# Performance work log

Measured on AMD Instinct MI355X. Metric: run time of the kernel, lower is better.

The kernel has to match this reference:

```python
import jax, jax.numpy as jnp
import numpy as np

B = 256          # graphs per batch
NPG = 512        # nodes per data graph
NG = B * NPG     # 131072 data-graph nodes
EG = NG * 8      # 1048576 data-graph edges
NQPG = 16        # nodes per query graph
NQ = B * NQPG    # 4096 query nodes
EQ = NQ * 8      # 32768 query edges
IN, H, L, OUT = 64, 128, 2, 1


def setup_inputs() -> dict:
    key = jax.random.key(0)
    ks = jax.random.split(key, 24)
    # edges constrained within each graph (offset + local index)
    g_off = jnp.repeat(jnp.arange(B, dtype=jnp.int32) * NPG, EG // B)
    q_off = jnp.repeat(jnp.arange(B, dtype=jnp.int32) * NQPG, EQ // B)
    inp = {
        "X": jax.random.normal(ks[0], (NG, IN), jnp.float32),
        "X_q": jax.random.normal(ks[1], (NQ, IN), jnp.float32),
        "g_src": g_off + jax.random.randint(ks[2], (EG,), 0, NPG, jnp.int32),
        "g_dst": g_off + jax.random.randint(ks[3], (EG,), 0, NPG, jnp.int32),
        "g_n2g": jnp.repeat(jnp.arange(B, dtype=jnp.int32), NPG),
        "q_src": q_off + jax.random.randint(ks[4], (EQ,), 0, NQPG, jnp.int32),
        "q_dst": q_off + jax.random.randint(ks[5], (EQ,), 0, NQPG, jnp.int32),
        "q_n2g": jnp.repeat(jnp.arange(B, dtype=jnp.int32), NQPG),
    }
    def lin(k, fi, fo):
        s = 1.0 / np.sqrt(fi)
        return jax.random.uniform(k, (fi, fo), jnp.float32, -s, s)
    inp["Wg"] = lin(ks[6], IN, H); inp["bg"] = jnp.zeros((H,), jnp.float32)
    inp["Wq"] = lin(ks[7], IN, H); inp["bq"] = jnp.zeros((H,), jnp.float32)
    inp["betas_g"] = jnp.ones((L,), jnp.float32)  # AGNN beta, init 1
    inp["betas_q"] = jnp.ones((L,), jnp.float32)
    inp["W1r"] = jnp.stack([lin(jax.random.fold_in(ks[8], l), 2 * H, H) for l in range(L)])
    inp["b1r"] = jnp.zeros((L, H), jnp.float32)
    inp["W2r"] = jnp.stack([lin(jax.random.fold_in(ks[9], l), H, H) for l in range(L)])
    inp["b2r"] = jnp.zeros((L, H), jnp.float32)
    inp["Wp1"] = lin(ks[10], H, H); inp["bp1"] = jnp.zeros((H,), jnp.float32)
    inp["Wp2"] = lin(ks[11], H, OUT); inp["bp2"] = jnp.zeros((OUT,), jnp.float32)
    return inp


def agnn(h, src, dst, beta, n):
    # DGL AGNNConv: edge logit = beta * cos(h_dst, h_src); softmax over in-edges of dst;
    # output_i = sum_j alpha_ij * h_j. Nodes with no in-edges get zeros.
    hn = h * jax.lax.rsqrt(jnp.sum(h * h, -1, keepdims=True) + 1e-24)
    e = beta * jnp.sum(hn[src] * hn[dst], -1)                      # [E]
    m = jax.ops.segment_max(e, dst, num_segments=n)
    m = jnp.where(jnp.isfinite(m), m, 0.0)
    ee = jnp.exp(e - m[dst])
    den = jax.ops.segment_sum(ee, dst, num_segments=n)             # [N]
    num = jax.ops.segment_sum(ee[:, None] * h[src], dst, num_segments=n)
    return jnp.where(den[:, None] > 0, num / jnp.maximum(den, 1e-24)[:, None], 0.0)


def reference(X, X_q, g_src, g_dst, g_n2g, q_src, q_dst, q_n2g,
              Wg, bg, Wq, bq, betas_g, betas_q, W1r, b1r, W2r, b2r,
              Wp1, bp1, Wp2, bp2):
    h_g = X @ Wg + bg              # [NG, H]
    h_q = X_q @ Wq + bq            # [NQ, H]
    for l in range(L):
        h_q = agnn(h_q, q_src, q_dst, betas_q[l], NQ)
        h_q_aggr = jax.ops.segment_sum(h_q, q_n2g, num_segments=B)        # dgl.sum_nodes -> [B, H]
        h_cat = jnp.concatenate([h_g, h_q_aggr[g_n2g]], axis=-1)          # per-node broadcast, [NG, 2H]
        h = agnn(h_cat, g_src, g_dst, betas_g[l], NG)                     # [NG, 2H]
        h_g = jax.nn.relu(h @ W1r[l] + b1r[l]) @ W2r[l] + b2r[l]          # MLP reduce -> [NG, H]
    hg_sum = jax.ops.segment_sum(h_g, g_n2g, num_segments=B)             # sum-pool per graph
    y = jax.nn.relu(hg_sum @ Wp1 + bp1) @ Wp2 + bp2                       # SumPredictor -> [B, OUT]
    return y
```

## Files before the change

kernel.cpp:

```cpp
#include <hip/hip_runtime.h>
#include <stdint.h>

#define B_   256
#define NPG  512
#define NG   131072
#define EPG  4096
#define NQPG 16
#define NQ   4096
#define EQPG 128
#define L_   2
#define HPITCH 136

typedef __attribute__((ext_vector_type(8))) short short8;
typedef __attribute__((ext_vector_type(4))) float floatx4;

__device__ inline float bf2f(unsigned short u){
    union { unsigned int i; float f; } x; x.i = ((unsigned int)u) << 16; return x.f;
}
__device__ inline unsigned short f2bf(float f){
    union { float f; unsigned int i; } x; x.f = f;
    unsigned int r = x.i + 0x7fff + ((x.i >> 16) & 1);
    return (unsigned short)(r >> 16);
}
__device__ inline float d2(unsigned int a, unsigned int b, float c){
#if __has_builtin(__builtin_amdgcn_fdot2_f32_bf16)
    typedef __attribute__((ext_vector_type(2))) __bf16 bf16x2;
    union { unsigned int u; bf16x2 v; } xa, xb;
    xa.u = a; xb.u = b;
    return __builtin_amdgcn_fdot2_f32_bf16(xa.v, xb.v, c, false);
#else
    union { unsigned int u; float f; } la, ha, lb, hb;
    la.u = a << 16; ha.u = a & 0xffff0000u;
    lb.u = b << 16; hb.u = b & 0xffff0000u;
    return fmaf(la.f, lb.f, fmaf(ha.f, hb.f, c));
#endif
}
__device__ inline float dot8(uint4 a, uint4 b){
    return d2(a.x,b.x, d2(a.y,b.y, d2(a.z,b.z, d2(a.w,b.w, 0.f))));
}
__device__ inline float dot8q(uint4 a, uint4 b, float c0){
    return d2(a.x,b.x, d2(a.y,b.y, d2(a.z,b.z, d2(a.w,b.w, c0))));
}

#if __has_builtin(__builtin_amdgcn_exp2f)
#define FEXP2(x) __builtin_amdgcn_exp2f(x)
#else
#define FEXP2(x) __expf((x) * 0.6931471805599453f)
#endif
#define LOG2E_ 1.4426950408889634f

__device__ inline float red16dpp(float v){
#if __has_builtin(__builtin_amdgcn_mov_dpp)
    int i;
    i = __builtin_amdgcn_mov_dpp(__float_as_int(v), 0xB1, 0xF, 0xF, true);
    v += __int_as_float(i);
    i = __builtin_amdgcn_mov_dpp(__float_as_int(v), 0x4E, 0xF, 0xF, true);
    v += __int_as_float(i);
    i = __builtin_amdgcn_mov_dpp(__float_as_int(v), 0x141, 0xF, 0xF, true);
    v += __int_as_float(i);
    i = __builtin_amdgcn_mov_dpp(__float_as_int(v), 0x128, 0xF, 0xF, true);
    v += __int_as_float(i);
    return v;
#else
    v += __shfl_xor(v,1); v += __shfl_xor(v,2);
    v += __shfl_xor(v,4); v += __shfl_xor(v,8);
    return v;
#endif
}

__device__ inline void red16dpp4(float& v0, float& v1, float& v2, float& v3){
#if defined(__gfx950__) || defined(__gfx942__) || defined(__gfx90a__)
    asm volatile(
        "s_nop 1\n\t"
        "v_add_f32_dpp %0, %0, %0 quad_perm:[1,0,3,2] row_mask:0xf bank_mask:0xf\n\t"
        "v_add_f32_dpp %1, %1, %1 quad_perm:[1,0,3,2] row_mask:0xf bank_mask:0xf\n\t"
        "v_add_f32_dpp %2, %2, %2 quad_perm:[1,0,3,2] row_mask:0xf bank_mask:0xf\n\t"
        "v_add_f32_dpp %3, %3, %3 quad_perm:[1,0,3,2] row_mask:0xf bank_mask:0xf\n\t"
        "v_add_f32_dpp %0, %0, %0 quad_perm:[2,3,0,1] row_mask:0xf bank_mask:0xf\n\t"
        "v_add_f32_dpp %1, %1, %1 quad_perm:[2,3,0,1] row_mask:0xf bank_mask:0xf\n\t"
        "v_add_f32_dpp %2, %2, %2 quad_perm:[2,3,0,1] row_mask:0xf bank_mask:0xf\n\t"
        "v_add_f32_dpp %3, %3, %3 quad_perm:[2,3,0,1] row_mask:0xf bank_mask:0xf\n\t"
        "v_add_f32_dpp %0, %0, %0 row_half_mirror row_mask:0xf bank_mask:0xf\n\t"
        "v_add_f32_dpp %1, %1, %1 row_half_mirror row_mask:0xf bank_mask:0xf\n\t"
        "v_add_f32_dpp %2, %2, %2 row_half_mirror row_mask:0xf bank_mask:0xf\n\t"
        "v_add_f32_dpp %3, %3, %3 row_half_mirror row_mask:0xf bank_mask:0xf\n\t"
        "v_add_f32_dpp %0, %0, %0 row_ror:8 row_mask:0xf bank_mask:0xf\n\t"
        "v_add_f32_dpp %1, %1, %1 row_ror:8 row_mask:0xf bank_mask:0xf\n\t"
        "v_add_f32_dpp %2, %2, %2 row_ror:8 row_mask:0xf bank_mask:0xf\n\t"
        "v_add_f32_dpp %3, %3, %3 row_ror:8 row_mask:0xf bank_mask:0xf"
        : "+v"(v0), "+v"(v1), "+v"(v2), "+v"(v3));
#else
    v0 = red16dpp(v0); v1 = red16dpp(v1); v2 = red16dpp(v2); v3 = red16dpp(v3);
#endif
}

#define ACCUM8(p0,p1,p2,p3,p4,p5,p6,p7,e,u) do { \
    p0 = fmaf(e, bf2f((unsigned short)((u).x&0xffffu)), p0); \
    p1 = fmaf(e, bf2f((unsigned short)((u).x>>16)),    p1); \
    p2 = fmaf(e, bf2f((unsigned short)((u).y&0xffffu)), p2); \
    p3 = fmaf(e, bf2f((unsigned short)((u).y>>16)),    p3); \
    p4 = fmaf(e, bf2f((unsigned short)((u).z&0xffffu)), p4); \
    p5 = fmaf(e, bf2f((unsigned short)((u).z>>16)),    p5); \
    p6 = fmaf(e, bf2f((unsigned short)((u).w&0xffffu)), p6); \
    p7 = fmaf(e, bf2f((unsigned short)((u).w>>16)),    p7); \
} while(0)

__global__ void k_transpose(const float* Wg, const float* Wq,
                            const float* W1r, const float* W2r,
                            unsigned short* WgT, unsigned short* WqT,
                            unsigned short* W1aT, unsigned short* W2rT){
    int idx = blockIdx.x*256 + threadIdx.x;
    if (idx < 8192){
        int k = idx >> 7, n = idx & 127; WgT[n*64 + k] = f2bf(Wg[idx]);
    } else if (idx < 16384){
        int i = idx - 8192; int k = i>>7, n = i&127; WqT[n*64+k] = f2bf(Wq[i]);
    } else if (idx < 49152){
        int i = idx - 16384; int l = i >> 14; int j = i & 16383; int k = j>>7, n = j&127;
        W1aT[l*16384 + n*128 + k] = f2bf(W1r[l*32768 + j]);
    } else {
        int i = idx - 49152; int l = i >> 14; int j = i & 16383; int k = j>>7, n = j&127;
        W2rT[l*16384 + n*128 + k] = f2bf(W2r[i]);
    }
}

__global__ __launch_bounds__(256) void k_csr(const int* __restrict__ g_src,
        const int* __restrict__ g_dst,
        unsigned short* __restrict__ csrc_g, int* __restrict__ off_g,
        float* __restrict__ degf, unsigned short* __restrict__ nodeperm){
    int g = blockIdx.x, t = threadIdx.x, lane = t & 63;
    __shared__ int cnt[NPG], woff[NPG];
    __shared__ int gscan[64];
    __shared__ int dh[64], dhoff[64];
    int gbase = g*NPG; size_t ebase = (size_t)g*EPG;
    for (int n=t;n<NPG;n+=256) cnt[n]=0;
    if (t<64) dh[t]=0;
    __syncthreads();
    for (int i=t;i<EPG;i+=256){
        int d = g_dst[ebase+i]-gbase;
        atomicAdd(&cnt[d],1);
    }
    __syncthreads();
    if (t < 64){
        int s=0;
        #pragma unroll
        for (int j=0;j<8;j++) s += cnt[t*8+j];
        int v=s;
        #pragma unroll
        for (int o=1;o<64;o<<=1){ int u=__shfl_up(v,o); if (lane>=o) v+=u; }
        gscan[t]=v;
    }
    __syncthreads();
    for (int n=t;n<NPG;n+=256){
        int grp=n>>3; int base = grp?gscan[grp-1]:0;
        for (int j=grp*8;j<n;j++) base+=cnt[j];
        off_g[g*NPG+n]=base; woff[n]=base;
        degf[gbase+n] = cnt[n]>0 ? 1.f : 0.f;
        atomicAdd(&dh[cnt[n] < 63 ? cnt[n] : 63], 1);
    }
    __syncthreads();
    if (t < 64){
        int v = dh[t];
        #pragma unroll
        for (int o=1;o<64;o<<=1){ int u=__shfl_up(v,o); if (lane>=o) v+=u; }
        dhoff[t] = v - dh[t];
    }
    __syncthreads();
    for (int n=t;n<NPG;n+=256){
        int d = cnt[n] < 63 ? cnt[n] : 63;
        int pos = atomicAdd(&dhoff[d],1);
        nodeperm[g*NPG+pos] = (unsigned short)n;
    }
    __syncthreads();
    for (int i=t;i<EPG;i+=256){
        int s = g_src[ebase+i]-gbase;
        int d = g_dst[ebase+i]-gbase;
        int pos = atomicAdd(&woff[d],1);
        csrc_g[ebase+pos]=(unsigned short)s;
    }
}

__global__ __launch_bounds__(256) void k_proj(const float* __restrict__ A,
        const unsigned short* __restrict__ Wt, const float* __restrict__ bias,
        unsigned short* __restrict__ out, float* __restrict__ invout,
        const float* __restrict__ Qv0){
    const int K = 64;
    int wave = threadIdx.x >> 6, lane = threadIdx.x & 63;
    int quad = lane >> 4, l16 = lane & 15;
    int wrow = blockIdx.x*64 + wave*16;
    floatx4 acc[8];
    #pragma unroll
    for (int t=0;t<8;t++){
        #pragma unroll
        for (int r=0;r<4;r++) acc[t][r]=0.f;
    }
    #pragma unroll
    for (int ks = 0; ks < 2; ks++){
        int koff = ks*32 + quad*8;
        const float* ap = A + (size_t)(wrow+l16)*K + koff;
        short8 a;
        #pragma unroll
        for (int j=0;j<8;j++) a[j] = (short)f2bf(ap[j]);
        #pragma unroll
        for (int t=0;t<8;t++){
            short8 b = *(const short8*)(Wt + (size_t)(t*16+l16)*K + koff);
            acc[t] = __builtin_amdgcn_mfma_f32_16x16x32_bf16(a, b, acc[t], 0,0,0);
        }
    }
    float ss[4] = {0.f,0.f,0.f,0.f};
    #pragma unroll
    for (int t=0;t<8;t++){
        int col = t*16 + l16;
        float bv = bias[col];
        #pragma unroll
        for (int r=0;r<4;r++){
            float v = acc[t][r] + bv;
            out[(size_t)(wrow + quad*4 + r)*128 + col] = f2bf(v);
            ss[r] += v*v;
        }
    }
    if (invout){
        #pragma unroll
        for (int r=0;r<4;r++){
            #pragma unroll
            for (int o=1;o<16;o<<=1) ss[r] += __shfl_xor(ss[r], o);
        }
        if (l16==0){
            #pragma unroll
            for (int r=0;r<4;r++){
                int row = wrow + quad*4 + r;
                invout[row] = rsqrtf(ss[r] + Qv0[row>>9] + 1e-24f);
            }
        }
    }
}

__global__ __launch_bounds__(256) void k_queryall(
        const unsigned short* __restrict__ h_q,
        const int* __restrict__ q_src, const int* __restrict__ q_dst,
        const float* __restrict__ betas_q,
        const float* __restrict__ W1r,
        float* __restrict__ Qv, float* __restrict__ cg2a){
    __shared__ unsigned short hqrows[NQPG*HPITCH];
    __shared__ float eq[EQPG];
    __shared__ unsigned short srcq[EQPG], dstq[EQPG];
    __shared__ float invq[NQPG], denq[NQPG], hqa[128], cg2s[128];
    __shared__ float QaccL;
    int g = blockIdx.x, t = threadIdx.x, sl = t & 15;
    {
        int row = t >> 4;
        *(uint4*)(hqrows + row*HPITCH + sl*8) =
            *(const uint4*)(h_q + (size_t)(g*NQPG+row)*128 + sl*8);
    }
    if (t < EQPG){
        srcq[t] = (unsigned short)(q_src[(size_t)g*EQPG+t] - g*NQPG);
        dstq[t] = (unsigned short)(q_dst[(size_t)g*EQPG+t] - g*NQPG);
    }
    int qn = t >> 4;
    for (int l=0; l<L_; l++){
        float beta_q = betas_q[l];
        if (t < NQPG) denq[t] = 0.f;
        if (t == 16) QaccL = 0.f;
        if (t >= 128 && t < 256) cg2s[t-128] = 0.f;
        __syncthreads();
        {
            uint4 u = *(const uint4*)(hqrows + qn*HPITCH + sl*8);
            float s = red16dpp(dot8(u,u));
            if (sl==0) invq[qn] = rsqrtf(s + 1e-24f);
        }
        __syncthreads();
        for (int e = qn; e < EQPG; e += 16){
            int s = srcq[e], d = dstq[e];
            uint4 us = *(const uint4*)(hqrows + s*HPITCH + sl*8);
            uint4 ud = *(const uint4*)(hqrows + d*HPITCH + sl*8);
            float v = red16dpp(dot8(us, ud));
            if (sl==0){
                float ee = __expf(beta_q * v * invq[s] * invq[d]);
                eq[e] = ee;
                atomicAdd(&denq[d], ee);
            }
        }
        __syncthreads();
        uint4 nq; nq.x=0; nq.y=0; nq.z=0; nq.w=0;
        {
            float wsum = denq[qn];
            if (wsum > 0.f){
                float a0=0,a1=0,a2=0,a3=0,a4=0,a5=0,a6=0,a7=0;
                for (int e=0;e<EQPG;e++){
                    if (dstq[e] == qn){
                        float wg = eq[e];
                        int s = srcq[e];
                        uint4 u = *(const uint4*)(hqrows + s*HPITCH + sl*8);
                        ACCUM8(a0,a1,a2,a3,a4,a5,a6,a7, wg, u);
                    }
                }
                float iw = __frcp_rn(wsum);
                nq.x = (unsigned int)f2bf(a0*iw) | ((unsigned int)f2bf(a1*iw)<<16);
                nq.y = (unsigned int)f2bf(a2*iw) | ((unsigned int)f2bf(a3*iw)<<16);
                nq.z = (unsigned int)f2bf(a4*iw) | ((unsigned int)f2bf(a5*iw)<<16);
                nq.w = (unsigned int)f2bf(a6*iw) | ((unsigned int)f2bf(a7*iw)<<16);
            }
        }
        __syncthreads();
        *(uint4*)(hqrows + qn*HPITCH + sl*8) = nq;
        __syncthreads();
        if (t < 128){
            float s = 0.f;
            for (int n=0;n<NQPG;n++) s += bf2f(hqrows[n*HPITCH + t]);
            hqa[t] = s;
            atomicAdd(&QaccL, s*s);
        }
        __syncthreads();
        if (t == 0) Qv[l*B_+g] = QaccL;
        {
            int jj = t & 127, kc = t >> 7;
            const float* Wl = W1r + (size_t)l*32768;
            float p = 0.f;
            for (int k = kc*64; k < kc*64+64; k++)
                p = fmaf(hqa[k], Wl[(size_t)(128+k)*128 + jj], p);
            atomicAdd(&cg2s[jj], p);
        }
        __syncthreads();
        if (t < 128) cg2a[((size_t)l*B_+g)*128 + t] = cg2s[t];
        __syncthreads();
    }
}

#define SMEM_GS 152592
__global__ __launch_bounds__(1024) void k_gstage(
        const unsigned short* __restrict__ h_g,
        const float* __restrict__ invg,
        const float* __restrict__ betag_p,
        const float* __restrict__ Qv_l,
        const unsigned short* __restrict__ csrc_g,
        const int* __restrict__ off_g,
        const unsigned short* __restrict__ nodeperm,
        unsigned short* __restrict__ aout){
    extern __shared__ __align__(16) char smem[];
    unsigned short* hrows = (unsigned short*)smem;
    float* inv            = (float*)(smem + 139264);
    unsigned short* ssrc  = (unsigned short*)(smem + 141312);
    int* offc             = (int*)(smem + 149504);
    unsigned short* nprm  = (unsigned short*)(smem + 151556);
    int g = blockIdx.x, t = threadIdx.x;
    int group = t >> 4, sl = t & 15;
    float beta_g = betag_p[0];
    int gbase = g*NPG;
    size_t ebase = (size_t)g*EPG;
    for (int i=t; i<8192; i+=1024){
        int row = i >> 4, col = i & 15;
        *(uint4*)(hrows + row*HPITCH + col*8) =
            *(const uint4*)(h_g + (size_t)(gbase+row)*128 + col*8);
    }
    for (int n=t; n<NPG; n+=1024){
        inv[n] = invg[gbase+n];
        nprm[n] = nodeperm[g*NPG+n];
    }
    for (int i=t; i<EPG; i+=1024) ssrc[i] = csrc_g[ebase+i];
    for (int n=t; n<=NPG; n+=1024) offc[n] = (n<NPG) ? off_g[g*NPG+n] : EPG;
    __syncthreads();
    float Q = Qv_l[g];
    float Qs = Q * 0.0625f;
    for (int idx = group; idx < NPG; idx += 64){
        int n = nprm[idx];
        int o = offc[n];
        int jend = offc[n+1];
        uint4 ov;
        if (jend > o){
            uint4 ud = *(const uint4*)(hrows + n*HPITCH + sl*8);
            float bn = beta_g * inv[n] * LOG2E_;
            float ws = 0.f;
            float a0=0,a1=0,a2=0,a3=0,a4=0,a5=0,a6=0,a7=0;
            int je1 = jend - 1;
            int p0 = ssrc[o];
            int p1 = ssrc[(o+1<je1)?o+1:je1];
            int p2 = ssrc[(o+2<je1)?o+2:je1];
            int p3 = ssrc[(o+3<je1)?o+3:je1];
            uint4 u0 = *(const uint4*)(hrows + p0*HPITCH + sl*8);
            uint4 u1 = *(const uint4*)(hrows + p1*HPITCH + sl*8);
            uint4 u2 = *(const uint4*)(hrows + p2*HPITCH + sl*8);
            uint4 u3 = *(const uint4*)(hrows + p3*HPITCH + sl*8);
            float i0 = inv[p0], i1 = inv[p1], i2 = inv[p2], i3 = inv[p3];
            for (int j = o; j < jend; j += 4){
                int q0 = (j+4<je1)?j+4:je1;
                int q1 = (j+5<je1)?j+5:je1;
                int q2 = (j+6<je1)?j+6:je1;
                int q3 = (j+7<je1)?j+7:je1;
                int s0 = ssrc[q0], s1 = ssrc[q1], s2 = ssrc[q2], s3 = ssrc[q3];
                uint4 n0 = *(const uint4*)(hrows + s0*HPITCH + sl*8);
                uint4 n1 = *(const uint4*)(hrows + s1*HPITCH + sl*8);
                uint4 n2 = *(const uint4*)(hrows + s2*HPITCH + sl*8);
                uint4 n3 = *(const uint4*)(hrows + s3*HPITCH + sl*8);
                float w0 = inv[s0], w1 = inv[s1], w2 = inv[s2], w3 = inv[s3];
                float v0 = dot8q(u0, ud, Qs);
                float v1 = dot8q(u1, ud, Qs);
                float v2 = dot8q(u2, ud, Qs);
                float v3 = dot8q(u3, ud, Qs);
                red16dpp4(v0, v1, v2, v3);
                float e0 = FEXP2(v0 * i0 * bn);
                float e1 = FEXP2(v1 * i1 * bn);
                float e2 = FEXP2(v2 * i2 * bn);
                float e3 = FEXP2(v3 * i3 * bn);
                if (j+1 >= jend) e1 = 0.f;
                if (j+2 >= jend) e2 = 0.f;
                if (j+3 >= jend) e3 = 0.f;
                ws += (e0 + e1) + (e2 + e3);
                ACCUM8(a0,a1,a2,a3,a4,a5,a6,a7, e0, u0);
                ACCUM8(a0,a1,a2,a3,a4,a5,a6,a7, e1, u1);
                ACCUM8(a0,a1,a2,a3,a4,a5,a6,a7, e2, u2);
                ACCUM8(a0,a1,a2,a3,a4,a5,a6,a7, e3, u3);
                u0 = n0; u1 = n1; u2 = n2; u3 = n3;
                i0 = w0; i1 = w1; i2 = w2; i3 = w3;
            }
            float iw = __frcp_rn(ws);
            ov.x = (unsigned int)f2bf(a0*iw) | ((unsigned int)f2bf(a1*iw)<<16);
            ov.y = (unsigned int)f2bf(a2*iw) | ((unsigned int)f2bf(a3*iw)<<16);
            ov.z = (unsigned int)f2bf(a4*iw) | ((unsigned int)f2bf(a5*iw)<<16);
            ov.w = (unsigned int)f2bf(a6*iw) | ((unsigned int)f2bf(a7*iw)<<16);
        } else {
            ov.x=0; ov.y=0; ov.z=0; ov.w=0;
        }
        *(uint4*)(aout + (size_t)(gbase+n)*128 + sl*8) = ov;
    }
}

#define SMEM_MLP (3*128*136*2)
__global__ __launch_bounds__(512, 2) void k_mlp_p(const unsigned short* __restrict__ A,
        const unsigned short* __restrict__ W1t, const float* __restrict__ b1,
        const float* __restrict__ cg2, const float* __restrict__ degf,
        const unsigned short* __restrict__ W2t, const float* __restrict__ b2,
        unsigned short* __restrict__ out, float* __restrict__ invout,
        const float* __restrict__ Qnext){
    extern __shared__ __align__(16) char smem[];
    unsigned short* W1s = (unsigned short*)smem;
    unsigned short* W2s = W1s + 128*136;
    unsigned short* h1  = W2s + 128*136;
    int t = threadIdx.x;
    int g = blockIdx.x;
    float Qn = Qnext ? Qnext[g] : 0.f;
    #pragma unroll
    for (int p=0;p<4;p++){
        int flat = p*4096 + t*8;
        int n = flat>>7, k = flat&127;
        *(uint4*)(W1s + n*136 + k) = *(const uint4*)(W1t + n*128 + k);
        *(uint4*)(W2s + n*136 + k) = *(const uint4*)(W2t + n*128 + k);
    }
    __syncthreads();
    int wave = t>>6, lane = t&63, quad = lane>>4, l16 = lane&15;
    const float* cg = cg2 + (size_t)g*128;
    short8 af[4];
    {
        int wrow = g*512 + wave*16;
        #pragma unroll
        for (int ks=0;ks<4;ks++)
            af[ks] = *(const short8*)(A + (size_t)(wrow+l16)*128 + ks*32 + quad*8);
    }
    for (int it=0; it<4; it++){
        int wrow = g*512 + it*128 + wave*16;
        floatx4 acc[8];
        #pragma unroll
        for (int t8=0;t8<8;t8++){
            #pragma unroll
            for (int r=0;r<4;r++) acc[t8][r]=0.f;
        }
        #pragma unroll
        for (int ks=0;ks<4;ks++){
            int koff = ks*32 + quad*8;
            #pragma unroll
            for (int t8=0;t8<8;t8++){
                short8 b = *(const short8*)(W1s + (t8*16+l16)*136 + koff);
                acc[t8] = __builtin_amdgcn_mfma_f32_16x16x32_bf16(af[ks], b, acc[t8], 0,0,0);
            }
        }
        float dg[4];
        #pragma unroll
        for (int r=0;r<4;r++) dg[r] = degf[wrow + quad*4 + r];
        #pragma unroll
        for (int t8=0;t8<8;t8++){
            int col = t8*16 + l16;
            float bv = b1[col];
            float cv = cg[col];
            #pragma unroll
            for (int r=0;r<4;r++){
                float v = acc[t8][r] + bv + dg[r]*cv;
                v = v > 0.f ? v : 0.f;
                h1[(wave*16 + quad*4 + r)*136 + col] = f2bf(v);
            }
        }
        __syncthreads();
        short8 afn[4];
        if (it < 3){
            int wrow_n = g*512 + (it+1)*128 + wave*16;
            #pragma unroll
            for (int ks=0;ks<4;ks++)
                afn[ks] = *(const short8*)(A + (size_t)(wrow_n+l16)*128 + ks*32 + quad*8);
        }
        short8 hf[4];
        #pragma unroll
        for (int ks=0;ks<4;ks++) hf[ks] = *(const short8*)(h1 + (wave*16+l16)*136 + ks*32 + quad*8);
        floatx4 acc2[8];
        #pragma unroll
        for (int t8=0;t8<8;t8++){
            #pragma unroll
            for (int r=0;r<4;r++) acc2[t8][r]=0.f;
        }
        #pragma unroll
        for (int ks=0;ks<4;ks++){
            int koff = ks*32 + quad*8;
            #pragma unroll
            for (int t8=0;t8<8;t8++){
                short8 b = *(const short8*)(W2s + (t8*16+l16)*136 + koff);
                acc2[t8] = __builtin_amdgcn_mfma_f32_16x16x32_bf16(hf[ks], b, acc2[t8], 0,0,0);
            }
        }
        float ss[4] = {0.f,0.f,0.f,0.f};
        #pragma unroll
        for (int t8=0;t8<8;t8++){
            int col = t8*16 + l16;
            float bv = b2[col];
            #pragma unroll
            for (int r=0;r<4;r++){
                float v = acc2[t8][r] + bv;
                out[(size_t)(wrow + quad*4 + r)*128 + col] = f2bf(v);
                ss[r] += v*v;
            }
        }
        if (Qnext){
            #pragma unroll
            for (int r=0;r<4;r++){
                #pragma unroll
                for (int o=1;o<16;o<<=1) ss[r] += __shfl_xor(ss[r], o);
            }
            if (l16==0){
                #pragma unroll
                for (int r=0;r<4;r++){
                    int row = wrow + quad*4 + r;
                    invout[row] = rsqrtf(ss[r] + Qn + 1e-24f);
                }
            }
        }
        __syncthreads();
        #pragma unroll
        for (int ks=0;ks<4;ks++) af[ks] = afn[ks];
    }
}

__global__ __launch_bounds__(512) void k_hgpred(const unsigned short* __restrict__ h_g,
        const float* __restrict__ Wp1, const float* __restrict__ bp1,
        const float* __restrict__ Wp2, const float* __restrict__ bp2,
        float* __restrict__ y){
    __shared__ float red[32][128];
    __shared__ float hsum[128];
    __shared__ float red2[128];
    int g = blockIdx.x, t = threadIdx.x;
    int c = t & 15, r0 = t >> 4;
    float s[8];
    #pragma unroll
    for (int k=0;k<8;k++) s[k]=0.f;
    for (int i=0;i<16;i++){
        int row = r0 + i*32;
        uint4 u = *(const uint4*)(h_g + (size_t)(g*NPG + row)*128 + c*8);
        s[0] += bf2f((unsigned short)(u.x&0xffff)); s[1] += bf2f((unsigned short)(u.x>>16));
        s[2] += bf2f((unsigned short)(u.y&0xffff)); s[3] += bf2f((unsigned short)(u.y>>16));
        s[4] += bf2f((unsigned short)(u.z&0xffff)); s[5] += bf2f((unsigned short)(u.z>>16));
        s[6] += bf2f((unsigned short)(u.w&0xffff)); s[7] += bf2f((unsigned short)(u.w>>16));
    }
    #pragma unroll
    for (int k=0;k<8;k++) red[r0][c*8+k] = s[k];
    __syncthreads();
    if (t < 128){
        float a = 0.f;
        #pragma unroll
        for (int r=0;r<32;r++) a += red[r][t];
        hsum[t] = a;
    }
    __syncthreads();
    if (t < 128){
        float acc = bp1[t];
        for (int k=0;k<128;k++) acc += hsum[k]*Wp1[k*128+t];
        acc = fmaxf(acc, 0.f);
        red2[t] = acc * Wp2[t];
    }
    __syncthreads();
    for (int s2=64; s2>0; s2>>=1){
        if (t<s2) red2[t]+=red2[t+s2];
        __syncthreads();
    }
    if (t==0) y[g] = red2[0] + bp2[0];
}

extern "C" void kernel_launch(void* const* d_in, const int* in_sizes, int n_in,
                              void* d_out, int out_size, void* d_ws, size_t ws_size,
                              hipStream_t stream) {
    const float* X    = (const float*)d_in[0];
    const float* X_q  = (const float*)d_in[1];
    const int* g_src = (const int*)d_in[2];
    const int* g_dst = (const int*)d_in[3];
    const int* q_src = (const int*)d_in[5];
    const int* q_dst = (const int*)d_in[6];
    const float* Wg   = (const float*)d_in[8];
    const float* bg   = (const float*)d_in[9];
    const float* Wq   = (const float*)d_in[10];
    const float* bq   = (const float*)d_in[11];
    const float* betas_g = (const float*)d_in[12];
    const float* betas_q = (const float*)d_in[13];
    const float* W1r  = (const float*)d_in[14];
    const float* b1r  = (const float*)d_in[15];
    const float* W2r  = (const float*)d_in[16];
    const float* b2r  = (const float*)d_in[17];
    const float* Wp1  = (const float*)d_in[18];
    const float* bp1  = (const float*)d_in[19];
    const float* Wp2  = (const float*)d_in[20];
    const float* bp2  = (const float*)d_in[21];

    uint8_t* w = (uint8_t*)d_ws;
    unsigned short* h_g  = (unsigned short*)w;    w += (size_t)NG*128*2;
    unsigned short* h_q  = (unsigned short*)w;    w += (size_t)NQ*128*2;
    unsigned short* aout = (unsigned short*)w;    w += (size_t)NG*128*2;
    float* invg  = (float*)w;                     w += (size_t)NG*4;
    float* degf  = (float*)w;                     w += (size_t)NG*4;
    float* Qv    = (float*)w;                     w += (size_t)L_*B_*4;
    float* cg2a  = (float*)w;                     w += (size_t)L_*B_*128*4;
    unsigned short* WgT   = (unsigned short*)w;   w += 8192*2;
    unsigned short* WqT   = (unsigned short*)w;   w += 8192*2;
    unsigned short* W1aT  = (unsigned short*)w;   w += 2*16384*2;
    unsigned short* W2rT  = (unsigned short*)w;   w += 2*16384*2;
    unsigned short* csrc_g = (unsigned short*)w;  w += (size_t)B_*EPG*2;
    unsigned short* nodeperm = (unsigned short*)w; w += (size_t)B_*NPG*2;
    int* off_g = (int*)w;                         w += (size_t)B_*NPG*4;

    static bool attr_done = false;
    if (!attr_done){
        hipFuncSetAttribute((const void*)k_mlp_p,
                            hipFuncAttributeMaxDynamicSharedMemorySize, SMEM_MLP);
        hipFuncSetAttribute((const void*)k_gstage,
                            hipFuncAttributeMaxDynamicSharedMemorySize, SMEM_GS);
        attr_done = true;
    }

    k_transpose<<<320,256,0,stream>>>(Wg,Wq,W1r,W2r,WgT,WqT,W1aT,W2rT);
    k_csr<<<B_,256,0,stream>>>(g_src,g_dst,csrc_g,off_g,degf,nodeperm);
    k_proj<<<NQ/64,256,0,stream>>>(X_q, WqT, bq, h_q, nullptr, nullptr);
    k_queryall<<<B_,256,0,stream>>>(h_q, q_src, q_dst, betas_q, W1r, Qv, cg2a);
    k_proj<<<NG/64,256,0,stream>>>(X, WgT, bg, h_g, invg, Qv);
    for (int l=0;l<L_;l++){
        k_gstage<<<B_,1024,SMEM_GS,stream>>>(h_g, invg, betas_g + l, Qv + l*B_,
                                             csrc_g, off_g, nodeperm, aout);
        k_mlp_p<<<B_,512,SMEM_MLP,stream>>>(aout, W1aT + l*16384, b1r + l*128,
                                            cg2a + (size_t)l*B_*128, degf,
                                            W2rT + l*16384, b2r + l*128, h_g,
                                            (l==0) ? invg : nullptr,
                                            (l==0) ? (Qv + B_) : nullptr);
    }
    k_hgpred<<<B_,512,0,stream>>>(h_g, Wp1, bp1, Wp2, bp2, (float*)d_out);
}
```

Measured before the change: 307.2 us.

## Fuse weight transpose, query projection and pooling/predictor into neighbouring kernels

Folds the weight-transpose kernel into the CSR-build kernel, computes the query projection inside the query kernel from X_q directly, and fuses the final sum-pool plus predictor MLP into the last MLP layer kernel so the final h_g is never written back. The gather loop in the graph stage is also restructured to prefetch source indices two iterations ahead. The goal is fewer launches and less global traffic. In exchange the query projection uses scalar FMAs with Wq read from global memory, and predictor work adds serial tail steps to the MLP kernel.

```diff
diff --git a/kernel.cpp b/kernel.cpp
--- a/kernel.cpp
+++ b/kernel.cpp
@@ -105,29 +105,28 @@
     p7 = fmaf(e, bf2f((unsigned short)((u).w>>16)),    p7); \
 } while(0)
 
-__global__ void k_transpose(const float* Wg, const float* Wq,
-                            const float* W1r, const float* W2r,
-                            unsigned short* WgT, unsigned short* WqT,
-                            unsigned short* W1aT, unsigned short* W2rT){
-    int idx = blockIdx.x*256 + threadIdx.x;
-    if (idx < 8192){
-        int k = idx >> 7, n = idx & 127; WgT[n*64 + k] = f2bf(Wg[idx]);
-    } else if (idx < 16384){
-        int i = idx - 8192; int k = i>>7, n = i&127; WqT[n*64+k] = f2bf(Wq[i]);
-    } else if (idx < 49152){
-        int i = idx - 16384; int l = i >> 14; int j = i & 16383; int k = j>>7, n = j&127;
-        W1aT[l*16384 + n*128 + k] = f2bf(W1r[l*32768 + j]);
-    } else {
-        int i = idx - 49152; int l = i >> 14; int j = i & 16383; int k = j>>7, n = j&127;
-        W2rT[l*16384 + n*128 + k] = f2bf(W2r[i]);
-    }
-}
-
-__global__ __launch_bounds__(256) void k_csr(const int* __restrict__ g_src,
+__global__ __launch_bounds__(256) void k_csrt(const int* __restrict__ g_src,
         const int* __restrict__ g_dst,
+        const float* __restrict__ Wg, const float* __restrict__ W1r,
+        const float* __restrict__ W2r,
+        unsigned short* __restrict__ WgT, unsigned short* __restrict__ W1aT,
+        unsigned short* __restrict__ W2rT,
         unsigned short* __restrict__ csrc_g, int* __restrict__ off_g,
         float* __restrict__ degf, unsigned short* __restrict__ nodeperm){
     int g = blockIdx.x, t = threadIdx.x, lane = t & 63;
+    for (int idx = g*256 + t; idx < 73728; idx += 65536){
+        if (idx < 8192){
+            int k = idx >> 7, n = idx & 127; WgT[n*64 + k] = f2bf(Wg[idx]);
+        } else if (idx < 40960){
+            int i = idx - 8192; int l = i >> 14; int j = i & 16383;
+            int k = j>>7, n = j&127;
+            W1aT[l*16384 + n*128 + k] = f2bf(W1r[l*32768 + j]);
+        } else {
+            int i = idx - 40960; int l = i >> 14; int j = i & 16383;
+            int k = j>>7, n = j&127;
+            W2rT[l*16384 + n*128 + k] = f2bf(W2r[i]);
+        }
+    }
     __shared__ int cnt[NPG], woff[NPG];
     __shared__ int gscan[64];
     __shared__ int dh[64], dhoff[64];
@@ -235,25 +234,42 @@
 }
 
 __global__ __launch_bounds__(256) void k_queryall(
-        const unsigned short* __restrict__ h_q,
+        const float* __restrict__ X_q,
+        const float* __restrict__ Wq, const float* __restrict__ bq,
         const int* __restrict__ q_src, const int* __restrict__ q_dst,
         const float* __restrict__ betas_q,
         const float* __restrict__ W1r,
         float* __restrict__ Qv, float* __restrict__ cg2a){
     __shared__ unsigned short hqrows[NQPG*HPITCH];
+    __shared__ float xq[NQPG*64];
     __shared__ float eq[EQPG];
     __shared__ unsigned short srcq[EQPG], dstq[EQPG];
     __shared__ float invq[NQPG], denq[NQPG], hqa[128], cg2s[128];
     __shared__ float QaccL;
     int g = blockIdx.x, t = threadIdx.x, sl = t & 15;
-    {
-        int row = t >> 4;
-        *(uint4*)(hqrows + row*HPITCH + sl*8) =
-            *(const uint4*)(h_q + (size_t)(g*NQPG+row)*128 + sl*8);
-    }
+    for (int i=t;i<NQPG*64;i+=256) xq[i] = X_q[(size_t)g*NQPG*64 + i];
     if (t < EQPG){
         srcq[t] = (unsigned short)(q_src[(size_t)g*EQPG+t] - g*NQPG);
         dstq[t] = (unsigned short)(q_dst[(size_t)g*EQPG+t] - g*NQPG);
+    }
+    __syncthreads();
+    {
+        int r = t >> 4, c0 = sl*8;
+        float v[8];
+        #pragma unroll
+        for (int j=0;j<8;j++) v[j] = bq[c0+j];
+        for (int k=0;k<64;k++){
+            float x = xq[r*64+k];
+            const float* wr = Wq + k*128 + c0;
+            #pragma unroll
+            for (int j=0;j<8;j++) v[j] = fmaf(x, wr[j], v[j]);
+        }
+        uint4 uu;
+        uu.x = (unsigned int)f2bf(v[0]) | ((unsigned int)f2bf(v[1])<<16);
+        uu.y = (unsigned int)f2bf(v[2]) | ((unsigned int)f2bf(v[3])<<16);
+        uu.z = (unsigned int)f2bf(v[4]) | ((unsigned int)f2bf(v[5])<<16);
+        uu.w = (unsigned int)f2bf(v[6]) | ((unsigned int)f2bf(v[7])<<16);
+        *(uint4*)(hqrows + r*HPITCH + sl*8) = uu;
     }
     int qn = t >> 4;
     for (int l=0; l<L_; l++){
@@ -326,6 +342,7 @@
 }
 
 #define SMEM_GS 152592
+#define CIDX(x) ((x) < je1 ? (x) : je1)
 __global__ __launch_bounds__(1024) void k_gstage(
         const unsigned short* __restrict__ h_g,
         const float* __restrict__ invg,
@@ -371,26 +388,29 @@
             float ws = 0.f;
             float a0=0,a1=0,a2=0,a3=0,a4=0,a5=0,a6=0,a7=0;
             int je1 = jend - 1;
-            int p0 = ssrc[o];
-            int p1 = ssrc[(o+1<je1)?o+1:je1];
-            int p2 = ssrc[(o+2<je1)?o+2:je1];
-            int p3 = ssrc[(o+3<je1)?o+3:je1];
-            uint4 u0 = *(const uint4*)(hrows + p0*HPITCH + sl*8);
-            uint4 u1 = *(const uint4*)(hrows + p1*HPITCH + sl*8);
-            uint4 u2 = *(const uint4*)(hrows + p2*HPITCH + sl*8);
-            uint4 u3 = *(const uint4*)(hrows + p3*HPITCH + sl*8);
-            float i0 = inv[p0], i1 = inv[p1], i2 = inv[p2], i3 = inv[p3];
+            int ia0 = ssrc[o];
+            int ia1 = ssrc[CIDX(o+1)];
+            int ia2 = ssrc[CIDX(o+2)];
+            int ia3 = ssrc[CIDX(o+3)];
+            uint4 u0 = *(const uint4*)(hrows + ia0*HPITCH + sl*8);
+            uint4 u1 = *(const uint4*)(hrows + ia1*HPITCH + sl*8);
+            uint4 u2 = *(const uint4*)(hrows + ia2*HPITCH + sl*8);
+            uint4 u3 = *(const uint4*)(hrows + ia3*HPITCH + sl*8);
+            float i0 = inv[ia0], i1 = inv[ia1], i2 = inv[ia2], i3 = inv[ia3];
+            int ib0 = ssrc[CIDX(o+4)];
+            int ib1 = ssrc[CIDX(o+5)];
+            int ib2 = ssrc[CIDX(o+6)];
+            int ib3 = ssrc[CIDX(o+7)];
             for (int j = o; j < jend; j += 4){
-                int q0 = (j+4<je1)?j+4:je1;
-                int q1 = (j+5<je1)?j+5:je1;
-                int q2 = (j+6<je1)?j+6:je1;
-                int q3 = (j+7<je1)?j+7:je1;
-                int s0 = ssrc[q0], s1 = ssrc[q1], s2 = ssrc[q2], s3 = ssrc[q3];
-                uint4 n0 = *(const uint4*)(hrows + s0*HPITCH + sl*8);
-                uint4 n1 = *(const uint4*)(hrows + s1*HPITCH + sl*8);
-                uint4 n2 = *(const uint4*)(hrows + s2*HPITCH + sl*8);
-                uint4 n3 = *(const uint4*)(hrows + s3*HPITCH + sl*8);
-                float w0 = inv[s0], w1 = inv[s1], w2 = inv[s2], w3 = inv[s3];
+                uint4 n0 = *(const uint4*)(hrows + ib0*HPITCH + sl*8);
+                uint4 n1 = *(const uint4*)(hrows + ib1*HPITCH + sl*8);
+                uint4 n2 = *(const uint4*)(hrows + ib2*HPITCH + sl*8);
+                uint4 n3 = *(const uint4*)(hrows + ib3*HPITCH + sl*8);
+                float w0 = inv[ib0], w1 = inv[ib1], w2 = inv[ib2], w3 = inv[ib3];
+                int ic0 = ssrc[CIDX(j+8)];
+                int ic1 = ssrc[CIDX(j+9)];
+                int ic2 = ssrc[CIDX(j+10)];
+                int ic3 = ssrc[CIDX(j+11)];
                 float v0 = dot8q(u0, ud, Qs);
                 float v1 = dot8q(u1, ud, Qs);
                 float v2 = dot8q(u2, ud, Qs);
@@ -410,6 +430,7 @@
                 ACCUM8(a0,a1,a2,a3,a4,a5,a6,a7, e3, u3);
                 u0 = n0; u1 = n1; u2 = n2; u3 = n3;
                 i0 = w0; i1 = w1; i2 = w2; i3 = w3;
+                ib0 = ic0; ib1 = ic1; ib2 = ic2; ib3 = ic3;
             }
             float iw = __frcp_rn(ws);
             ov.x = (unsigned int)f2bf(a0*iw) | ((unsigned int)f2bf(a1*iw)<<16);
@@ -423,17 +444,22 @@
     }
 }
 
-#define SMEM_MLP (3*128*136*2)
+#define SMEM_MLP (3*128*136*2 + 1024)
 __global__ __launch_bounds__(512, 2) void k_mlp_p(const unsigned short* __restrict__ A,
         const unsigned short* __restrict__ W1t, const float* __restrict__ b1,
         const float* __restrict__ cg2, const float* __restrict__ degf,
         const unsigned short* __restrict__ W2t, const float* __restrict__ b2,
         unsigned short* __restrict__ out, float* __restrict__ invout,
-        const float* __restrict__ Qnext){
+        const float* __restrict__ Qnext,
+        const float* __restrict__ Wp1, const float* __restrict__ bp1,
+        const float* __restrict__ Wp2, const float* __restrict__ bp2,
+        float* __restrict__ y){
     extern __shared__ __align__(16) char smem[];
     unsigned short* W1s = (unsigned short*)smem;
     unsigned short* W2s = W1s + 128*136;
     unsigned short* h1  = W2s + 128*136;
+    float* hsum = (float*)(smem + 3*128*136*2);
+    float* red2 = hsum + 128;
     int t = threadIdx.x;
     int g = blockIdx.x;
     float Qn = Qnext ? Qnext[g] : 0.f;
@@ -444,9 +470,13 @@
         *(uint4*)(W1s + n*136 + k) = *(const uint4*)(W1t + n*128 + k);
         *(uint4*)(W2s + n*136 + k) = *(const uint4*)(W2t + n*128 + k);
     }
+    if (y && t < 128) hsum[t] = 0.f;
     __syncthreads();
     int wave = t>>6, lane = t&63, quad = lane>>4, l16 = lane&15;
     const float* cg = cg2 + (size_t)g*128;
+    float psum[8];
+    #pragma unroll
+    for (int j=0;j<8;j++) psum[j] = 0.f;
     short8 af[4];
     {
         int wrow = g*512 + wave*16;
@@ -520,7 +550,11 @@
             #pragma unroll
             for (int r=0;r<4;r++){
                 float v = acc2[t8][r] + bv;
-                out[(size_t)(wrow + quad*4 + r)*128 + col] = f2bf(v);
+                if (y){
+                    psum[t8] += v;
+                } else {
+                    out[(size_t)(wrow + quad*4 + r)*128 + col] = f2bf(v);
+                }
                 ss[r] += v*v;
             }
         }
@@ -542,50 +576,30 @@
         #pragma unroll
         for (int ks=0;ks<4;ks++) af[ks] = afn[ks];
     }
-}
-
-__global__ __launch_bounds__(512) void k_hgpred(const unsigned short* __restrict__ h_g,
-        const float* __restrict__ Wp1, const float* __restrict__ bp1,
-        const float* __restrict__ Wp2, const float* __restrict__ bp2,
-        float* __restrict__ y){
-    __shared__ float red[32][128];
-    __shared__ float hsum[128];
-    __shared__ float red2[128];
-    int g = blockIdx.x, t = threadIdx.x;
-    int c = t & 15, r0 = t >> 4;
-    float s[8];
-    #pragma unroll
-    for (int k=0;k<8;k++) s[k]=0.f;
-    for (int i=0;i<16;i++){
-        int row = r0 + i*32;
-        uint4 u = *(const uint4*)(h_g + (size_t)(g*NPG + row)*128 + c*8);
-        s[0] += bf2f((unsigned short)(u.x&0xffff)); s[1] += bf2f((unsigned short)(u.x>>16));
-        s[2] += bf2f((unsigned short)(u.y&0xffff)); s[3] += bf2f((unsigned short)(u.y>>16));
-        s[4] += bf2f((unsigned short)(u.z&0xffff)); s[5] += bf2f((unsigned short)(u.z>>16));
-        s[6] += bf2f((unsigned short)(u.w&0xffff)); s[7] += bf2f((unsigned short)(u.w>>16));
-    }
-    #pragma unroll
-    for (int k=0;k<8;k++) red[r0][c*8+k] = s[k];
-    __syncthreads();
-    if (t < 128){
-        float a = 0.f;
-        #pragma unroll
-        for (int r=0;r<32;r++) a += red[r][t];
-        hsum[t] = a;
-    }
-    __syncthreads();
-    if (t < 128){
-        float acc = bp1[t];
-        for (int k=0;k<128;k++) acc += hsum[k]*Wp1[k*128+t];
-        acc = fmaxf(acc, 0.f);
-        red2[t] = acc * Wp2[t];
-    }
-    __syncthreads();
-    for (int s2=64; s2>0; s2>>=1){
-        if (t<s2) red2[t]+=red2[t+s2];
-        __syncthreads();
-    }
-    if (t==0) y[g] = red2[0] + bp2[0];
+    if (y){
+        #pragma unroll
+        for (int j=0;j<8;j++){
+            psum[j] += __shfl_xor(psum[j], 16);
+            psum[j] += __shfl_xor(psum[j], 32);
+        }
+        if (lane < 16){
+            #pragma unroll
+            for (int j=0;j<8;j++) atomicAdd(&hsum[j*16 + lane], psum[j]);
+        }
+        __syncthreads();
+        if (t < 128){
+            float acc = bp1[t];
+            for (int k=0;k<128;k++) acc += hsum[k]*Wp1[k*128+t];
+            acc = fmaxf(acc, 0.f);
+            red2[t] = acc * Wp2[t];
+        }
+        __syncthreads();
+        for (int s2=64; s2>0; s2>>=1){
+            if (t<s2) red2[t]+=red2[t+s2];
+            __syncthreads();
+        }
+        if (t==0) y[g] = red2[0] + bp2[0];
+    }
 }
 
 extern "C" void kernel_launch(void* const* d_in, const int* in_sizes, int n_in,
@@ -614,14 +628,12 @@
 
     uint8_t* w = (uint8_t*)d_ws;
     unsigned short* h_g  = (unsigned short*)w;    w += (size_t)NG*128*2;
-    unsigned short* h_q  = (unsigned short*)w;    w += (size_t)NQ*128*2;
     unsigned short* aout = (unsigned short*)w;    w += (size_t)NG*128*2;
     float* invg  = (float*)w;                     w += (size_t)NG*4;
     float* degf  = (float*)w;                     w += (size_t)NG*4;
     float* Qv    = (float*)w;                     w += (size_t)L_*B_*4;
     float* cg2a  = (float*)w;                     w += (size_t)L_*B_*128*4;
     unsigned short* WgT   = (unsigned short*)w;   w += 8192*2;
-    unsigned short* WqT   = (unsigned short*)w;   w += 8192*2;
     unsigned short* W1aT  = (unsigned short*)w;   w += 2*16384*2;
     unsigned short* W2rT  = (unsigned short*)w;   w += 2*16384*2;
     unsigned short* csrc_g = (unsigned short*)w;  w += (size_t)B_*EPG*2;
@@ -637,10 +649,11 @@
         attr_done = true;
     }
 
-    k_transpose<<<320,256,0,stream>>>(Wg,Wq,W1r,W2r,WgT,WqT,W1aT,W2rT);
-    k_csr<<<B_,256,0,stream>>>(g_src,g_dst,csrc_g,off_g,degf,nodeperm);
-    k_proj<<<NQ/64,256,0,stream>>>(X_q, WqT, bq, h_q, nullptr, nullptr);
-    k_queryall<<<B_,256,0,stream>>>(h_q, q_src, q_dst, betas_q, W1r, Qv, cg2a);
+    k_csrt<<<B_,256,0,stream>>>(g_src, g_dst, Wg, W1r, W2r,
+                                WgT, W1aT, W2rT,
+                                csrc_g, off_g, degf, nodeperm);
+    k_queryall<<<B_,256,0,stream>>>(X_q, Wq, bq, q_src, q_dst, betas_q, W1r,
+                                    Qv, cg2a);
     k_proj<<<NG/64,256,0,stream>>>(X, WgT, bg, h_g, invg, Qv);
     for (int l=0;l<L_;l++){
         k_gstage<<<B_,1024,SMEM_GS,stream>>>(h_g, invg, betas_g + l, Qv + l*B_,
@@ -649,7 +662,8 @@
                                             cg2a + (size_t)l*B_*128, degf,
                                             W2rT + l*16384, b2r + l*128, h_g,
                                             (l==0) ? invg : nullptr,
-                                            (l==0) ? (Qv + B_) : nullptr);
-    }
-    k_hgpred<<<B_,512,0,stream>>>(h_g, Wp1, bp1, Wp2, bp2, (float*)d_out);
-}
+                                            (l==0) ? (Qv + B_) : nullptr,
+                                            Wp1, bp1, Wp2, bp2,
+                                            (l==L_-1) ? (float*)d_out : nullptr);
+    }
+}
```

After: 305.4 us. Within noise of the previous version (-0.6%).
